# Kernel optimization log

Measured on AMD Instinct MI355X. Metric: run time of the kernel, lower is better.

The kernel has to match this reference:

```python
import jax, jax.numpy as jnp
import numpy as np

NUM_GRAPHS = 16384


def setup_inputs() -> dict:
    key = jax.random.key(0)
    k1, k2, k3, k4 = jax.random.split(key, 4)
    N, C = 1000000, 128
    x = jax.random.normal(k1, (N, C), dtype=jnp.float32)
    batch = jnp.sort(jax.random.randint(k2, (N,), 0, NUM_GRAPHS)).astype(jnp.int64)
    # Linear weights, kaiming-ish scale
    gate_w = jax.random.normal(k3, (C, 1), dtype=jnp.float32) * (1.0 / np.sqrt(C))
    gate_b = jnp.zeros((1,), dtype=jnp.float32)
    nn_w = jax.random.normal(k4, (C, 2 * C), dtype=jnp.float32) * (1.0 / np.sqrt(C))
    nn_b = jnp.zeros((2 * C,), dtype=jnp.float32)
    return {"x": x, "batch": batch, "gate_w": gate_w, "gate_b": gate_b,
            "nn_w": nn_w, "nn_b": nn_b}


def reference(x, batch, gate_w, gate_b, nn_w, nn_b):
    # gate_nn: [N, C] -> [N, 1]
    gate = (x @ gate_w + gate_b)[:, 0]            # [N]
    # nn: [N, C] -> [N, 2C]
    h = x @ nn_w + nn_b                           # [N, 2C]
    # per-graph (segment) softmax over gate scores
    m = jax.ops.segment_max(gate, batch, num_segments=NUM_GRAPHS)   # [B]
    e = jnp.exp(gate - m[batch])                                    # [N]
    s = jax.ops.segment_sum(e, batch, num_segments=NUM_GRAPHS)      # [B]
    w = e / s[batch]                                                # [N]
    # weighted scatter-sum: [B, 2C]
    out = jax.ops.segment_sum(h * w[:, None], batch, num_segments=NUM_GRAPHS)
    return out
```

## Files before the change

kernel.cpp:

```cpp
#include <hip/hip_runtime.h>

#define NUM_GRAPHS 16384
#define C 128
#define WAVE_ROWS 128
#define G 16

__global__ __launch_bounds__(256) void gate_accum_kernel(
    const float* __restrict__ x,
    const int*   __restrict__ batch,
    const float* __restrict__ gate_w,
    float*       __restrict__ y,
    float*       __restrict__ s,
    int N)
{
    const int wave = (blockIdx.x * blockDim.x + threadIdx.x) >> 6;
    const int lane = threadIdx.x & 63;

    long long r0 = (long long)wave * WAVE_ROWS;
    if (r0 >= N) return;
    long long r1 = r0 + WAVE_ROWS;
    if (r1 > N) r1 = N;

    const float gw0 = gate_w[lane * 2];
    const float gw1 = gate_w[lane * 2 + 1];
    const float2* __restrict__ x2 = (const float2*)x;

    float acc0 = 0.f, acc1 = 0.f, se = 0.f;
    int cur = batch[r0];

    for (long long r = r0; r < r1; ++r) {
        int b = batch[r];
        if (b != cur) {
            atomicAdd(&y[(long long)cur * C + lane * 2], acc0);
            atomicAdd(&y[(long long)cur * C + lane * 2 + 1], acc1);
            if (lane == 0) atomicAdd(&s[cur], se);
            acc0 = acc1 = se = 0.f;
            cur = b;
        }
        float2 xv = x2[r * 64 + lane];
        float p = xv.x * gw0 + xv.y * gw1;
        #pragma unroll
        for (int off = 32; off > 0; off >>= 1)
            p += __shfl_xor(p, off, 64);
        float e = __expf(p);
        acc0 += e * xv.x;
        acc1 += e * xv.y;
        se   += e;
    }
    atomicAdd(&y[(long long)cur * C + lane * 2], acc0);
    atomicAdd(&y[(long long)cur * C + lane * 2 + 1], acc1);
    if (lane == 0) atomicAdd(&s[cur], se);
}

__global__ __launch_bounds__(256) void finalize_kernel(
    const float* __restrict__ y,
    const float* __restrict__ s,
    const float* __restrict__ nn_w,
    const float* __restrict__ nn_b,
    float*       __restrict__ out)
{
    const int j  = threadIdx.x;
    const int b0 = blockIdx.x * G;

    __shared__ float ysh[G * C];
    __shared__ float ssh[G];

    for (int idx = threadIdx.x; idx < G * C; idx += 256) {
        int g = idx >> 7;
        float sv = s[b0 + g];
        ysh[idx] = (sv > 0.f) ? y[(long long)b0 * C + idx] / sv : 0.f;
    }
    if (threadIdx.x < G) ssh[threadIdx.x] = s[b0 + threadIdx.x];
    __syncthreads();

    float acc[G];
    #pragma unroll
    for (int g = 0; g < G; ++g) acc[g] = 0.f;

    #pragma unroll 4
    for (int c = 0; c < C; ++c) {
        float wv = nn_w[c * 256 + j];
        #pragma unroll
        for (int g = 0; g < G; ++g)
            acc[g] += ysh[g * C + c] * wv;
    }

    const float bias = nn_b[j];
    #pragma unroll
    for (int g = 0; g < G; ++g)
        out[(long long)(b0 + g) * 256 + j] = (ssh[g] > 0.f) ? acc[g] + bias : 0.f;
}

extern "C" void kernel_launch(void* const* d_in, const int* in_sizes, int n_in,
                              void* d_out, int out_size, void* d_ws, size_t ws_size,
                              hipStream_t stream) {
    const float* x      = (const float*)d_in[0];
    const int*   batch  = (const int*)d_in[1];
    const float* gate_w = (const float*)d_in[2];
    const float* nn_w   = (const float*)d_in[4];
    const float* nn_b   = (const float*)d_in[5];
    float* out = (float*)d_out;
    const int N = in_sizes[1];

    float* y = (float*)d_ws;
    float* s = y + (size_t)NUM_GRAPHS * C;

    hipMemsetAsync(d_ws, 0,
                   ((size_t)NUM_GRAPHS * C + NUM_GRAPHS) * sizeof(float),
                   stream);

    const int n_waves = (N + WAVE_ROWS - 1) / WAVE_ROWS;
    const int blocks  = (n_waves + 3) / 4;
    gate_accum_kernel<<<blocks, 256, 0, stream>>>(x, batch, gate_w, y, s, N);

    finalize_kernel<<<NUM_GRAPHS / G, 256, 0, stream>>>(y, s, nn_w, nn_b, out);
}
```

Before: 759.1 us.

## Process four rows per wave with 16-lane groups and float4 loads

The gate-accumulate kernel now splits each wave into four 16-lane groups, each handling every fourth row with two float4 loads per lane. The gate dot-product reduction needs four shuffle steps instead of six, and each row load is wider. This exposes more memory-level parallelism per wave and cuts the serial per-row dependency. In exchange, the four groups keep separate accumulators, so segment flushes issue more atomics. Each lane also holds eight accumulators, which raises register use.

```diff
diff --git a/kernel.cpp b/kernel.cpp
--- a/kernel.cpp
+++ b/kernel.cpp
@@ -15,41 +15,57 @@
 {
     const int wave = (blockIdx.x * blockDim.x + threadIdx.x) >> 6;
     const int lane = threadIdx.x & 63;
+    const int g    = lane >> 4;
+    const int t    = lane & 15;
 
-    long long r0 = (long long)wave * WAVE_ROWS;
+    int r0 = wave * WAVE_ROWS;
     if (r0 >= N) return;
-    long long r1 = r0 + WAVE_ROWS;
-    if (r1 > N) r1 = N;
+    int r1 = min(r0 + WAVE_ROWS, N);
 
-    const float gw0 = gate_w[lane * 2];
-    const float gw1 = gate_w[lane * 2 + 1];
-    const float2* __restrict__ x2 = (const float2*)x;
+    const float4* __restrict__ gw4 = (const float4*)(gate_w + t * 8);
+    const float4 gwa = gw4[0];
+    const float4 gwb = gw4[1];
 
-    float acc0 = 0.f, acc1 = 0.f, se = 0.f;
-    int cur = batch[r0];
+    float acc[8] = {0.f, 0.f, 0.f, 0.f, 0.f, 0.f, 0.f, 0.f};
+    float se = 0.f;
+    int cur = batch[min(r0 + g, r1 - 1)];
 
-    for (long long r = r0; r < r1; ++r) {
-        int b = batch[r];
-        if (b != cur) {
-            atomicAdd(&y[(long long)cur * C + lane * 2], acc0);
-            atomicAdd(&y[(long long)cur * C + lane * 2 + 1], acc1);
-            if (lane == 0) atomicAdd(&s[cur], se);
-            acc0 = acc1 = se = 0.f;
-            cur = b;
+    for (int r = r0 + g; r < r1; r += 4) {
+        const float4* __restrict__ xp = (const float4*)(x + (size_t)r * C + t * 8);
+        float4 a = xp[0];
+        float4 b = xp[1];
+        int bb = batch[r];
+
+        float p = a.x * gwa.x + a.y * gwa.y + a.z * gwa.z + a.w * gwa.w
+                + b.x * gwb.x + b.y * gwb.y + b.z * gwb.z + b.w * gwb.w;
+        p += __shfl_xor(p, 1, 64);
+        p += __shfl_xor(p, 2, 64);
+        p += __shfl_xor(p, 4, 64);
+        p += __shfl_xor(p, 8, 64);
+        float e = __expf(p);
+
+        if (bb != cur) {
+            #pragma unroll
+            for (int k = 0; k < 8; ++k)
+                atomicAdd(&y[cur * C + t * 8 + k], acc[k]);
+            if (t == 0) atomicAdd(&s[cur], se);
+            #pragma unroll
+            for (int k = 0; k < 8; ++k) acc[k] = 0.f;
+            se = 0.f;
+            cur = bb;
         }
-        float2 xv = x2[r * 64 + lane];
-        float p = xv.x * gw0 + xv.y * gw1;
-        #pragma unroll
-        for (int off = 32; off > 0; off >>= 1)
-            p += __shfl_xor(p, off, 64);
-        float e = __expf(p);
-        acc0 += e * xv.x;
-        acc1 += e * xv.y;
-        se   += e;
+
+        acc[0] += e * a.x; acc[1] += e * a.y;
+        acc[2] += e * a.z; acc[3] += e * a.w;
+        acc[4] += e * b.x; acc[5] += e * b.y;
+        acc[6] += e * b.z; acc[7] += e * b.w;
+        se += e;
     }
-    atomicAdd(&y[(long long)cur * C + lane * 2], acc0);
-    atomicAdd(&y[(long long)cur * C + lane * 2 + 1], acc1);
-    if (lane == 0) atomicAdd(&s[cur], se);
+
+    #pragma unroll
+    for (int k = 0; k < 8; ++k)
+        atomicAdd(&y[cur * C + t * 8 + k], acc[k]);
+    if (t == 0) atomicAdd(&s[cur], se);
 }
 
 __global__ __launch_bounds__(256) void finalize_kernel(
@@ -66,29 +82,29 @@
     __shared__ float ssh[G];
 
     for (int idx = threadIdx.x; idx < G * C; idx += 256) {
-        int g = idx >> 7;
-        float sv = s[b0 + g];
-        ysh[idx] = (sv > 0.f) ? y[(long long)b0 * C + idx] / sv : 0.f;
+        int gg = idx >> 7;
+        float sv = s[b0 + gg];
+        ysh[idx] = (sv > 0.f) ? y[(size_t)b0 * C + idx] / sv : 0.f;
     }
     if (threadIdx.x < G) ssh[threadIdx.x] = s[b0 + threadIdx.x];
     __syncthreads();
 
     float acc[G];
     #pragma unroll
-    for (int g = 0; g < G; ++g) acc[g] = 0.f;
+    for (int gg = 0; gg < G; ++gg) acc[gg] = 0.f;
 
     #pragma unroll 4
     for (int c = 0; c < C; ++c) {
         float wv = nn_w[c * 256 + j];
         #pragma unroll
-        for (int g = 0; g < G; ++g)
-            acc[g] += ysh[g * C + c] * wv;
+        for (int gg = 0; gg < G; ++gg)
+            acc[gg] += ysh[gg * C + c] * wv;
     }
 
     const float bias = nn_b[j];
     #pragma unroll
-    for (int g = 0; g < G; ++g)
-        out[(long long)(b0 + g) * 256 + j] = (ssh[g] > 0.f) ? acc[g] + bias : 0.f;
+    for (int gg = 0; gg < G; ++gg)
+        out[(size_t)(b0 + gg) * 256 + j] = (ssh[gg] > 0.f) ? acc[gg] + bias : 0.f;
 }
 
 extern "C" void kernel_launch(void* const* d_in, const int* in_sizes, int n_in,
```

Measured after the change: 1.014 ms. +33.5%, slower.
